# Kernel optimization log

Hardware: AMD Instinct MI355X
Metric: run time of the kernel (lower is better)

The kernel has to match this reference:

```python
import jax, jax.numpy as jnp
import numpy as np

BATCH, T, H, S, P, NH = 4, 2048, 1024, 64, 64, 8
HD = H // NH

def setup_inputs() -> dict:
    key = jax.random.key(0)
    ks = jax.random.split(key, 16)
    sH = 1.0 / np.sqrt(H)
    d = {}
    d["builder_state"] = jax.random.normal(ks[0], (BATCH, T, H), jnp.float32)
    d["base_state"] = jax.random.normal(ks[1], (BATCH, T, H), jnp.float32)
    d["input_ids"] = jax.random.randint(ks[2], (BATCH, T), 0, 32000)
    d["program_probs"] = jax.random.uniform(ks[3], (BATCH, T, P), jnp.float32)
    # SSM params (scaled from raw randn for numerical stability of the 2048-step recurrence)
    d["A"] = jax.random.normal(ks[4], (S, S), jnp.float32) * (0.5 / np.sqrt(S))
    d["Bmat"] = jax.random.normal(ks[5], (H, S), jnp.float32) * sH
    d["Cmat"] = jax.random.normal(ks[6], (S, H), jnp.float32) * (1.0 / np.sqrt(S))
    d["W_in"] = jax.random.normal(ks[7], (H, H), jnp.float32) * sH
    d["b_in"] = jnp.zeros((H,), jnp.float32)
    d["W_qkv"] = jax.random.normal(ks[8], (3 * H, H), jnp.float32) * sH
    d["b_qkv"] = jnp.zeros((3 * H,), jnp.float32)
    d["W_o"] = jax.random.normal(ks[9], (H, H), jnp.float32) * sH
    d["b_o"] = jnp.zeros((H,), jnp.float32)
    d["W_prog"] = jax.random.normal(ks[10], (H, P), jnp.float32) * (1.0 / np.sqrt(P))
    d["b_prog"] = jnp.zeros((H,), jnp.float32)
    d["g1"] = jnp.ones((H,), jnp.float32); d["beta1"] = jnp.zeros((H,), jnp.float32)
    d["g2"] = jnp.ones((H,), jnp.float32); d["beta2"] = jnp.zeros((H,), jnp.float32)
    return d

def _layernorm(x, g, b):
    mu = jnp.mean(x, axis=-1, keepdims=True)
    var = jnp.mean((x - mu) ** 2, axis=-1, keepdims=True)
    return (x - mu) * jax.lax.rsqrt(var + 1e-5) * g + b

def _mha(q_in, kv_in, W_qkv, b_qkv, W_o, b_o):
    Wq, Wk, Wv = jnp.split(W_qkv, 3, axis=0)
    bq, bk, bv = jnp.split(b_qkv, 3, axis=0)
    def heads(x, W, b):  # [B,T,H] -> [B,NH,T,HD]
        y = x @ W.T + b
        return y.reshape(y.shape[0], y.shape[1], NH, HD).transpose(0, 2, 1, 3)
    q, k, v = heads(q_in, Wq, bq), heads(kv_in, Wk, bk), heads(kv_in, Wv, bv)
    scores = jnp.einsum('bhqd,bhkd->bhqk', q, k) * (1.0 / np.sqrt(HD))
    attn = jax.nn.softmax(scores, axis=-1)
    out = jnp.einsum('bhqk,bhkd->bhqd', attn, v)
    out = out.transpose(0, 2, 1, 3).reshape(q_in.shape)
    return out @ W_o.T + b_o

def reference(builder_state, base_state, input_ids, program_probs,
              A, Bmat, Cmat, W_in, b_in, W_qkv, b_qkv, W_o, b_o,
              W_prog, b_prog, g1, beta1, g2, beta2):
    # cross-attention sublayer (norm1 shared between builder and base states)
    residual = builder_state
    x = _layernorm(builder_state, g1, beta1)
    base_n = _layernorm(base_state, g1, beta1)
    x = residual + _mha(x, base_n, W_qkv, b_qkv, W_o, b_o)
    # SSM sublayer: state_{t} = silu(A @ state_{t-1}) + B^T u_t ; y_t = state_t @ C
    residual = x
    xn = _layernorm(x, g2, beta2)
    U = (xn @ W_in.T + b_in) @ Bmat            # [B,T,S] precomputed input drive
    def step(s, u_t):                           # s: [B,S], u_t: [B,S]
        s = jax.nn.silu(s @ A.T) + u_t
        return s, s
    _, states = jax.lax.scan(step, jnp.zeros((builder_state.shape[0], S), U.dtype),
                             U.transpose(1, 0, 2))  # states: [T,B,S]
    ssm_out = jnp.einsum('tbs,sh->bth', states, Cmat)
    x = residual + ssm_out
    # program modulation
    mod = program_probs.mean(axis=1) @ W_prog.T + b_prog   # [B,H]
    return x + mod[:, None, :]
```

## Files before the change

### kernel.cpp

```cpp
#include <hip/hip_runtime.h>
#include <cstdint>
#include <cstddef>

typedef unsigned short u16;
typedef short bf16x8 __attribute__((ext_vector_type(8)));
typedef float f32x4 __attribute__((ext_vector_type(4)));
typedef u16 u16x4 __attribute__((ext_vector_type(4)));
typedef u16 u16x8 __attribute__((ext_vector_type(8)));

#define DEVFN static __device__ __forceinline__

DEVFN u16 f32_to_bf16(float f){
  unsigned u = __float_as_uint(f);
  u += 0x7fffu + ((u >> 16) & 1u);
  return (u16)(u >> 16);
}

DEVFN f32x4 mfma16(bf16x8 a, bf16x8 b, f32x4 c){
  return __builtin_amdgcn_mfma_f32_16x16x32_bf16(a, b, c, 0, 0, 0);
}

DEVFN void gload_lds16(const void* g, void* l){
  __builtin_amdgcn_global_load_lds(
      (const __attribute__((address_space(1))) void*)g,
      (__attribute__((address_space(3))) void*)l, 16, 0, 0);
}

__global__ __launch_bounds__(256,1) void prep_kernel(
    const float* __restrict__ W_qkv, const float* __restrict__ W_o,
    const float* __restrict__ Cm, const float* __restrict__ W_in,
    const float* __restrict__ Bm, const float* __restrict__ b_in,
    const float* __restrict__ pp,
    u16* __restrict__ Wq16, u16* __restrict__ Wo16, u16* __restrict__ CmT,
    u16* __restrict__ WcT, float* __restrict__ ub, float* __restrict__ partial)
{
  const int blk = blockIdx.x;
  if (blk < 1024){
    for (int i = blk*256 + threadIdx.x; i < 786432; i += 1024*256){
      float4 v = ((const float4*)W_qkv)[i];
      u16x4 o; o[0]=f32_to_bf16(v.x); o[1]=f32_to_bf16(v.y); o[2]=f32_to_bf16(v.z); o[3]=f32_to_bf16(v.w);
      ((u16x4*)Wq16)[i] = o;
    }
  } else if (blk < 1280){
    for (int i = (blk-1024)*256 + threadIdx.x; i < 262144; i += 256*256){
      float4 v = ((const float4*)W_o)[i];
      u16x4 o; o[0]=f32_to_bf16(v.x); o[1]=f32_to_bf16(v.y); o[2]=f32_to_bf16(v.z); o[3]=f32_to_bf16(v.w);
      ((u16x4*)Wo16)[i] = o;
    }
  } else if (blk < 1536){
    int i = (blk-1280)*256 + threadIdx.x;
    int h = i >> 6, s = i & 63;
    CmT[i] = f32_to_bf16(Cm[s*1024 + h]);
  } else if (blk < 1792){
    int b2 = blk - 1536;
    const int kl = threadIdx.x & 63, sl = threadIdx.x >> 6;
    const int k = ((b2 & 15) << 6) + kl;
    const int s = ((b2 >> 4) << 2) + sl;
    float a = 0.f;
#pragma unroll 8
    for (int jj = 0; jj < 1024; jj++) a = fmaf(W_in[jj*1024 + k], Bm[jj*64 + s], a);
    WcT[s*1024 + k] = f32_to_bf16(a);
  } else if (blk == 1792){
    if (threadIdx.x < 64){
      const int s = threadIdx.x;
      float a = 0.f;
      for (int jj = 0; jj < 1024; jj++) a = fmaf(b_in[jj], Bm[jj*64 + s], a);
      ub[s] = a;
    }
  } else {
    const int idx = blk - 1793;
    const int c = idx & 31, b = idx >> 5, t = threadIdx.x;
    const int p = t & 63, g = t >> 6;
    const float* basep = pp + (size_t)b*2048*64 + (size_t)c*64*64;
    float s = 0.f;
#pragma unroll
    for (int i = g*16; i < g*16 + 16; i++) s += basep[i*64 + p];
    __shared__ float red[256];
    red[t] = s;
    __syncthreads();
    if (t < 64) partial[(b*32 + c)*64 + t] = (red[t] + red[64+t]) + (red[128+t] + red[192+t]);
  }
}

DEVFN void ln_row(const float* __restrict__ srcrow, u16* __restrict__ dstrow,
                  const float* __restrict__ g, const float* __restrict__ beta, int t)
{
  const float4 v = ((const float4*)srcrow)[t];
  float s1 = v.x+v.y+v.z+v.w;
  float s2 = v.x*v.x+v.y*v.y+v.z*v.z+v.w*v.w;
#pragma unroll
  for (int off = 32; off > 0; off >>= 1){ s1 += __shfl_xor(s1, off); s2 += __shfl_xor(s2, off); }
  __shared__ float w1[4], w2[4];
  if ((t & 63) == 0){ w1[t>>6] = s1; w2[t>>6] = s2; }
  __syncthreads();
  s1 = (w1[0]+w1[1])+(w1[2]+w1[3]);
  s2 = (w2[0]+w2[1])+(w2[2]+w2[3]);
  const float mean = s1*(1.f/1024.f);
  const float var  = s2*(1.f/1024.f) - mean*mean;
  const float rstd = rsqrtf(var + 1e-5f);
  const float4 gv = ((const float4*)g)[t];
  const float4 bv = ((const float4*)beta)[t];
  u16x4 o;
  o[0] = f32_to_bf16((v.x-mean)*rstd*gv.x + bv.x);
  o[1] = f32_to_bf16((v.y-mean)*rstd*gv.y + bv.y);
  o[2] = f32_to_bf16((v.z-mean)*rstd*gv.z + bv.z);
  o[3] = f32_to_bf16((v.w-mean)*rstd*gv.w + bv.w);
  *(u16x4*)&dstrow[t*4] = o;
}

__global__ __launch_bounds__(256,1) void ln_bf16_kernel(
    const float* __restrict__ src, u16* __restrict__ dst,
    const float* __restrict__ g, const float* __restrict__ beta)
{
  const int row = blockIdx.x;
  ln_row(src + (size_t)row*1024, dst + (size_t)row*1024, g, beta, threadIdx.x);
}

__global__ __launch_bounds__(256,1) void ln2x_bf16_kernel(
    const float* __restrict__ src0, u16* __restrict__ dst0,
    const float* __restrict__ src1, u16* __restrict__ dst1,
    const float* __restrict__ g, const float* __restrict__ beta)
{
  int row = blockIdx.x;
  if (row < 8192) ln_row(src0 + (size_t)row*1024, dst0 + (size_t)row*1024, g, beta, threadIdx.x);
  else { row -= 8192; ln_row(src1 + (size_t)row*1024, dst1 + (size_t)row*1024, g, beta, threadIdx.x); }
}

template<int BM,int BN,int WM,int WN,int MT,int NT,int EPI>
__global__ __launch_bounds__(256,1) void gemm_bt(
    const u16* __restrict__ Ag, const u16* __restrict__ Bg,
    void* __restrict__ Cout, const float* __restrict__ bias,
    const float* __restrict__ resid, const float* __restrict__ modv,
    int M, int N, int K)
{
  static_assert(BM == WM*MT*16 && BN == WN*NT*16 && WM*WN == 4, "tile config");
  __shared__ u16 As[BM*64];
  __shared__ u16 Bs[BN*64];
  const int t = threadIdx.x;
  const int lane = t & 63, wave = t >> 6;
  const int wm = wave / WN, wn = wave % WN;
  const int lrow = lane & 15, lq = lane >> 4;
  const int m0 = blockIdx.y * BM, n0 = blockIdx.x * BN;

  f32x4 acc[MT][NT];
#pragma unroll
  for (int i = 0; i < MT; i++)
#pragma unroll
    for (int j = 0; j < NT; j++){ acc[i][j][0]=0.f; acc[i][j][1]=0.f; acc[i][j][2]=0.f; acc[i][j][3]=0.f; }

  for (int kt = 0; kt < K; kt += 64){
#pragma unroll
    for (int i = 0; i < BM/32; i++){
      int idx = (i*4 + wave)*64 + lane;
      int r = idx >> 3, s = idx & 7;
      int c = s ^ (r & 7);
      gload_lds16(&Ag[(size_t)(m0 + r)*K + kt + c*8], &As[(size_t)(i*4 + wave)*64*8]);
    }
#pragma unroll
    for (int i = 0; i < BN/32; i++){
      int idx = (i*4 + wave)*64 + lane;
      int r = idx >> 3, s = idx & 7;
      int c = s ^ (r & 7);
      gload_lds16(&Bg[(size_t)(n0 + r)*K + kt + c*8], &Bs[(size_t)(i*4 + wave)*64*8]);
    }
    __syncthreads();
#pragma unroll
    for (int kk = 0; kk < 2; kk++){
      bf16x8 af[MT], bfr[NT];
      const int sl = (kk*4 + lq) ^ (lrow & 7);
#pragma unroll
      for (int mt = 0; mt < MT; mt++)
        af[mt] = *(const bf16x8*)&As[(wm*MT*16 + mt*16 + lrow)*64 + sl*8];
#pragma unroll
      for (int nt = 0; nt < NT; nt++)
        bfr[nt] = *(const bf16x8*)&Bs[(wn*NT*16 + nt*16 + lrow)*64 + sl*8];
#pragma unroll
      for (int mt = 0; mt < MT; mt++)
#pragma unroll
        for (int nt = 0; nt < NT; nt++)
          acc[mt][nt] = mfma16(af[mt], bfr[nt], acc[mt][nt]);
    }
    __syncthreads();
  }
  const int rb = m0 + wm*MT*16;
  const int cb = n0 + wn*NT*16;
#pragma unroll
  for (int mt = 0; mt < MT; mt++){
#pragma unroll
    for (int nt = 0; nt < NT; nt++){
#pragma unroll
      for (int r = 0; r < 4; r++){
        int row = rb + mt*16 + lq*4 + r;
        int col = cb + nt*16 + lrow;
        float v = acc[mt][nt][r];
        if (EPI & 2) v += bias[col];
        if (EPI & 4) v += resid[(size_t)row*N + col];
        if (EPI & 8) v += modv[(row >> 11)*1024 + col];
        if (EPI & 1) ((u16*)Cout)[(size_t)row*N + col] = f32_to_bf16(v);
        else         ((float*)Cout)[(size_t)row*N + col] = v;
      }
    }
  }
}

__global__ __launch_bounds__(256,1) void gemm_qkv(
    const u16* __restrict__ QNa, const u16* __restrict__ KVNa,
    const u16* __restrict__ Wq, u16* __restrict__ Qb, u16* __restrict__ KVb,
    const float* __restrict__ bias)
{
  const int bid = blockIdx.x;
  const u16* Ag; const u16* Bg; u16* Cout; const float* bp;
  int N, m0, n0; float scale;
  if (bid < 512){
    Ag = QNa; Bg = Wq; Cout = Qb; bp = bias; N = 1024;
    m0 = (bid >> 3) * 128; n0 = (bid & 7) * 128;
    scale = 0.08838834764831845f * 1.4426950408889634f;
  } else {
    int b2 = bid - 512;
    Ag = KVNa; Bg = Wq + 1024*1024; Cout = KVb; bp = bias + 1024; N = 2048;
    m0 = (b2 >> 4) * 128; n0 = (b2 & 15) * 128;
    scale = 1.0f;
  }
  const int K = 1024;
  __shared__ u16 As[128*64];
  __shared__ u16 Bs[128*64];
  const int t = threadIdx.x;
  const int lane = t & 63, wave = t >> 6;
  const int wm = wave >> 1, wn = wave & 1;
  const int lrow = lane & 15, lq = lane >> 4;

  f32x4 acc[4][4];
#pragma unroll
  for (int i = 0; i < 4; i++)
#pragma unroll
    for (int j = 0; j < 4; j++){ acc[i][j][0]=0.f; acc[i][j][1]=0.f; acc[i][j][2]=0.f; acc[i][j][3]=0.f; }

  for (int kt = 0; kt < K; kt += 64){
#pragma unroll
    for (int i = 0; i < 4; i++){
      int idx = (i*4 + wave)*64 + lane;
      int r = idx >> 3, s = idx & 7;
      int c = s ^ (r & 7);
      gload_lds16(&Ag[(size_t)(m0 + r)*K + kt + c*8], &As[(size_t)(i*4 + wave)*64*8]);
    }
#pragma unroll
    for (int i = 0; i < 4; i++){
      int idx = (i*4 + wave)*64 + lane;
      int r = idx >> 3, s = idx & 7;
      int c = s ^ (r & 7);
      gload_lds16(&Bg[(size_t)(n0 + r)*K + kt + c*8], &Bs[(size_t)(i*4 + wave)*64*8]);
    }
    __syncthreads();
#pragma unroll
    for (int kk = 0; kk < 2; kk++){
      bf16x8 af[4], bfr[4];
      const int sl = (kk*4 + lq) ^ (lrow & 7);
#pragma unroll
      for (int mt = 0; mt < 4; mt++)
        af[mt] = *(const bf16x8*)&As[(wm*64 + mt*16 + lrow)*64 + sl*8];
#pragma unroll
      for (int nt = 0; nt < 4; nt++)
        bfr[nt] = *(const bf16x8*)&Bs[(wn*64 + nt*16 + lrow)*64 + sl*8];
#pragma unroll
      for (int mt = 0; mt < 4; mt++)
#pragma unroll
        for (int nt = 0; nt < 4; nt++)
          acc[mt][nt] = mfma16(af[mt], bfr[nt], acc[mt][nt]);
    }
    __syncthreads();
  }
  const int rb = m0 + wm*64;
  const int cb = n0 + wn*64;
#pragma unroll
  for (int mt = 0; mt < 4; mt++){
#pragma unroll
    for (int nt = 0; nt < 4; nt++){
#pragma unroll
      for (int r = 0; r < 4; r++){
        int row = rb + mt*16 + lq*4 + r;
        int col = cb + nt*16 + lrow;
        float v = (acc[mt][nt][r] + bp[col]) * scale;
        Cout[(size_t)row*N + col] = f32_to_bf16(v);
      }
    }
  }
}

__global__ __launch_bounds__(512,1) void flash_attn(
    const u16* __restrict__ Qb, const u16* __restrict__ KVb, u16* __restrict__ Ob)
{
  __shared__ u16 Ks[64*128];
  __shared__ unsigned Vt2[128*34];
  __shared__ u16 Ps[8][16*68];
  const int t = threadIdx.x;
  const int lane = t & 63, wave = t >> 6;
  const int lrow = lane & 15, lq = lane >> 4;
  const int b = blockIdx.y >> 3, h = blockIdx.y & 7;
  const int q0 = blockIdx.x * 128;

  bf16x8 qf[4];
  {
    int grow = b*2048 + q0 + wave*16 + lrow;
#pragma unroll
    for (int ks = 0; ks < 4; ks++)
      qf[ks] = *(const bf16x8*)&Qb[(size_t)grow*1024 + h*128 + ks*32 + lq*8];
  }
  float lsum[4] = {0.f,0.f,0.f,0.f};
  f32x4 Oa[8];
#pragma unroll
  for (int i = 0; i < 8; i++){ Oa[i][0]=0.f; Oa[i][1]=0.f; Oa[i][2]=0.f; Oa[i][3]=0.f; }

  const int key_k = t >> 3, cg = t & 7;
  const int kp = t & 31, dg = t >> 5;

  const size_t KSTEP = (size_t)64*2048;
  const u16* Kpg = &KVb[(size_t)(b*2048 + key_k)*2048 + h*128];
  const u16* Vpg = &KVb[(size_t)(b*2048 + kp*2)*2048 + h*128 + 1024 + dg*8];

  u16x8 kreg[2];
  u16x8 vreg[2];

#pragma unroll
  for (int i = 0; i < 2; i++) kreg[i] = *(const u16x8*)&Kpg[(cg*2+i)*8];
  vreg[0] = *(const u16x8*)&Vpg[0];
  vreg[1] = *(const u16x8*)&Vpg[2048];
#pragma unroll
  for (int i = 0; i < 2; i++){
    int ch = cg*2 + i;
    int ph = ch ^ (key_k & 7);
    *(u16x8*)&Ks[key_k*128 + ph*8] = kreg[i];
  }
#pragma unroll
  for (int jj = 0; jj < 8; jj++)
    Vt2[(dg*8+jj)*34 + kp] = (unsigned)vreg[0][jj] | ((unsigned)vreg[1][jj] << 16);

  for (int kt = 0; kt < 32; kt++){
    __syncthreads();
    if (kt < 31){
      const u16* kpg = Kpg + (size_t)(kt+1)*KSTEP;
#pragma unroll
      for (int i = 0; i < 2; i++) kreg[i] = *(const u16x8*)&kpg[(cg*2+i)*8];
      const u16* vg = Vpg + (size_t)(kt+1)*KSTEP;
      vreg[0] = *(const u16x8*)&vg[0];
      vreg[1] = *(const u16x8*)&vg[2048];
    }

    f32x4 sacc[4];
    __builtin_amdgcn_s_setprio(1);
#pragma unroll
    for (int nt = 0; nt < 4; nt++){
      f32x4 a; a[0]=0.f; a[1]=0.f; a[2]=0.f; a[3]=0.f;
#pragma unroll
      for (int ks = 0; ks < 4; ks++){
        int ph = (ks*4 + lq) ^ (lrow & 7);
        bf16x8 kf = *(const bf16x8*)&Ks[(nt*16+lrow)*128 + ph*8];
        a = mfma16(qf[ks], kf, a);
      }
      sacc[nt] = a;
    }
    __builtin_amdgcn_s_setprio(0);
#pragma unroll
    for (int nt = 0; nt < 4; nt++)
#pragma unroll
      for (int r = 0; r < 4; r++){
        float p = exp2f(sacc[nt][r]);
        lsum[r] += p;
        Ps[wave][(lq*4+r)*68 + nt*16 + lrow] = f32_to_bf16(p);
      }
    __builtin_amdgcn_s_setprio(1);
#pragma unroll
    for (int ks2 = 0; ks2 < 2; ks2++){
      bf16x8 pa;
      ((u16x4*)&pa)[0] = *(const u16x4*)&Ps[wave][lrow*68 + ks2*32 + lq*8];
      ((u16x4*)&pa)[1] = *(const u16x4*)&Ps[wave][lrow*68 + ks2*32 + lq*8 + 4];
#pragma unroll
      for (int nt2 = 0; nt2 < 8; nt2++){
        bf16x8 vf;
        int dwoff = (nt2*16+lrow)*34 + ks2*16 + lq*4;
        ((uint2*)&vf)[0] = *(const uint2*)&Vt2[dwoff];
        ((uint2*)&vf)[1] = *(const uint2*)&Vt2[dwoff+2];
        Oa[nt2] = mfma16(pa, vf, Oa[nt2]);
      }
    }
    __builtin_amdgcn_s_setprio(0);
    __syncthreads();
    if (kt < 31){
#pragma unroll
      for (int i = 0; i < 2; i++){
        int ch = cg*2 + i;
        int ph = ch ^ (key_k & 7);
        *(u16x8*)&Ks[key_k*128 + ph*8] = kreg[i];
      }
#pragma unroll
      for (int jj = 0; jj < 8; jj++)
        Vt2[(dg*8+jj)*34 + kp] = (unsigned)vreg[0][jj] | ((unsigned)vreg[1][jj] << 16);
    }
  }
#pragma unroll
  for (int r = 0; r < 4; r++){
#pragma unroll
    for (int off = 1; off < 16; off <<= 1) lsum[r] += __shfl_xor(lsum[r], off);
  }
  float inv[4];
#pragma unroll
  for (int r = 0; r < 4; r++) inv[r] = 1.0f / lsum[r];
  const int growb = b*2048 + q0 + wave*16;
#pragma unroll
  for (int nt2 = 0; nt2 < 8; nt2++)
#pragma unroll
    for (int r = 0; r < 4; r++){
      float o = Oa[nt2][r]*inv[r];
      Ob[(size_t)(growb + lq*4 + r)*1024 + h*128 + nt2*16 + lrow] = f32_to_bf16(o);
    }
}

__global__ __launch_bounds__(64,1) void scan_chunk_kernel(
    const float* __restrict__ U, const float* __restrict__ A, u16* __restrict__ S,
    const float* __restrict__ partial, const float* __restrict__ Wp,
    const float* __restrict__ bp, float* __restrict__ mo)
{
  const int b = blockIdx.y, c = blockIdx.x, j = threadIdx.x;
  if (c == 64){
    float s = 0.f;
#pragma unroll
    for (int cc = 0; cc < 32; cc++) s += partial[(b*32 + cc)*64 + j];
    __shared__ float pms[64];
    pms[j] = s * (1.f/2048.f);
    __syncthreads();
    for (int jo = 0; jo < 16; jo++){
      int hc = jo*64 + j;
      float a = bp[hc];
#pragma unroll 8
      for (int q = 0; q < 64; q++) a = fmaf(pms[q], Wp[hc*64+q], a);
      mo[b*1024 + hc] = a;
    }
    return;
  }
  float Ar[64];
#pragma unroll
  for (int k = 0; k < 64; k++) Ar[k] = A[j*64 + k];
  const float* Ub = U + (size_t)b*2048*64;
  u16* Sb = S + (size_t)b*2048*64;
  const int tout = c*32;
  const int tend = tout + 32;
  int t0 = tout - 48; if (t0 < 0) t0 = 0;
  __shared__ float sbuf[2][64];
  sbuf[0][j] = 0.f;
  __syncthreads();
  float unext = Ub[t0*64 + j];
  const float NLOG2E = -1.4426950408889634f;
  for (int t = t0; t < tend; t++){
    const int cur = (t - t0) & 1;
    f32x4 sv[16];
#pragma unroll
    for (int r = 0; r < 16; r++) sv[r] = *((const f32x4*)&sbuf[cur][r*4]);
    float u = unext;
    int tn = t + 1; if (tn >= tend) tn = tend - 1;
    unext = Ub[tn*64 + j];
    float a0=0.f, a1=0.f, a2=0.f, a3=0.f;
#pragma unroll
    for (int r = 0; r < 16; r++){
      a0 = fmaf(Ar[4*r+0], sv[r][0], a0);
      a1 = fmaf(Ar[4*r+1], sv[r][1], a1);
      a2 = fmaf(Ar[4*r+2], sv[r][2], a2);
      a3 = fmaf(Ar[4*r+3], sv[r][3], a3);
    }
    float y = (a0+a1)+(a2+a3);
    float e = exp2f(y*NLOG2E);
    float s = fmaf(y, __builtin_amdgcn_rcpf(1.f + e), u);
    sbuf[cur^1][j] = s;
    if (t >= tout) Sb[t*64 + j] = f32_to_bf16(s);
  }
}

extern "C" void kernel_launch(void* const* d_in, const int* in_sizes, int n_in,
                              void* d_out, int out_size, void* d_ws, size_t ws_size,
                              hipStream_t stream)
{
  (void)in_sizes; (void)n_in; (void)out_size; (void)ws_size;
  const float* builder = (const float*)d_in[0];
  const float* base    = (const float*)d_in[1];
  const float* pp      = (const float*)d_in[3];
  const float* Amat    = (const float*)d_in[4];
  const float* Bmat    = (const float*)d_in[5];
  const float* Cmat    = (const float*)d_in[6];
  const float* W_in    = (const float*)d_in[7];
  const float* b_in    = (const float*)d_in[8];
  const float* W_qkv   = (const float*)d_in[9];
  const float* b_qkv   = (const float*)d_in[10];
  const float* W_o     = (const float*)d_in[11];
  const float* b_o     = (const float*)d_in[12];
  const float* W_prog  = (const float*)d_in[13];
  const float* b_prog  = (const float*)d_in[14];
  const float* g1      = (const float*)d_in[15];
  const float* beta1   = (const float*)d_in[16];
  const float* g2      = (const float*)d_in[17];
  const float* beta2   = (const float*)d_in[18];
  float* out = (float*)d_out;

  char* ws = (char*)d_ws;
  const size_t MB = (size_t)1 << 20;
  u16*   Qb   = (u16*)  (ws + 0*MB);
  u16*   KVb  = (u16*)  (ws + 16*MB);
  float* Xf   = (float*)(ws + 48*MB);
  u16*   QN   = (u16*)  (ws + 80*MB);
  u16*   KVN  = (u16*)  (ws + 96*MB);
  u16*   Wq16 = (u16*)  (ws + 112*MB);
  u16*   Wo16 = (u16*)  (ws + 118*MB);
  u16*   WcT  = (u16*)  (ws + 120*MB);
  u16*   CmT  = (u16*)  (ws + 120*MB + 256*1024);
  float* Uf   = (float*)(ws + 121*MB);
  u16*   Sb   = (u16*)  (ws + 123*MB);
  float* ub   = (float*)(ws + 124*MB);
  float* modv = (float*)(ws + 124*MB + 8192);
  float* ppart= (float*)(ws + 124*MB + 32768);

  prep_kernel<<<1921,256,0,stream>>>(W_qkv, W_o, Cmat, W_in, Bmat, b_in, pp,
                                     Wq16, Wo16, CmT, WcT, ub, ppart);

  ln2x_bf16_kernel<<<16384,256,0,stream>>>(builder, QN, base, KVN, g1, beta1);

  gemm_qkv<<<1536,256,0,stream>>>(QN, KVN, Wq16, Qb, KVb, b_qkv);

  flash_attn<<<dim3(16,32),512,0,stream>>>(Qb, KVb, QN);

  gemm_bt<128,128,2,2,4,4,6><<<dim3(8,64),256,0,stream>>>(QN, Wo16, Xf, b_o, builder, nullptr, 8192,1024,1024);

  ln_bf16_kernel<<<8192,256,0,stream>>>(Xf, KVN, g2, beta2);

  gemm_bt<64,64,2,2,2,2,2><<<dim3(1,128),256,0,stream>>>(KVN, WcT, Uf, ub, nullptr, nullptr, 8192,64,1024);

  scan_chunk_kernel<<<dim3(65,4),64,0,stream>>>(Uf, Amat, Sb, ppart, W_prog, b_prog, modv);

  gemm_bt<128,128,2,2,4,4,12><<<dim3(8,64),256,0,stream>>>(Sb, CmT, out, nullptr, Xf, modv, 8192,1024,64);
}
```

Measured before the change: 511.9 us.

## Rewrite flash attention with 32x32 MFMA and in-register P via permlane swap

```diff
diff --git a/kernel.cpp b/kernel.cpp
--- a/kernel.cpp
+++ b/kernel.cpp
@@ -5,6 +5,7 @@
 typedef unsigned short u16;
 typedef short bf16x8 __attribute__((ext_vector_type(8)));
 typedef float f32x4 __attribute__((ext_vector_type(4)));
+typedef float f32x16 __attribute__((ext_vector_type(16)));
 typedef u16 u16x4 __attribute__((ext_vector_type(4)));
 typedef u16 u16x8 __attribute__((ext_vector_type(8)));
 
@@ -18,6 +19,10 @@
 
 DEVFN f32x4 mfma16(bf16x8 a, bf16x8 b, f32x4 c){
   return __builtin_amdgcn_mfma_f32_16x16x32_bf16(a, b, c, 0, 0, 0);
+}
+
+DEVFN f32x16 mfma32(bf16x8 a, bf16x8 b, f32x16 c){
+  return __builtin_amdgcn_mfma_f32_32x32x16_bf16(a, b, c, 0, 0, 0);
 }
 
 DEVFN void gload_lds16(const void* g, void* l){
@@ -286,131 +291,162 @@
   }
 }
 
-__global__ __launch_bounds__(512,1) void flash_attn(
+__global__ __launch_bounds__(256,1) void flash_attn(
     const u16* __restrict__ Qb, const u16* __restrict__ KVb, u16* __restrict__ Ob)
 {
   __shared__ u16 Ks[64*128];
   __shared__ unsigned Vt2[128*34];
-  __shared__ u16 Ps[8][16*68];
   const int t = threadIdx.x;
   const int lane = t & 63, wave = t >> 6;
-  const int lrow = lane & 15, lq = lane >> 4;
+  const int l31 = lane & 31, hi = lane >> 5;
   const int b = blockIdx.y >> 3, h = blockIdx.y & 7;
   const int q0 = blockIdx.x * 128;
 
-  bf16x8 qf[4];
+  bf16x8 qf[8];
   {
-    int grow = b*2048 + q0 + wave*16 + lrow;
-#pragma unroll
-    for (int ks = 0; ks < 4; ks++)
-      qf[ks] = *(const bf16x8*)&Qb[(size_t)grow*1024 + h*128 + ks*32 + lq*8];
-  }
-  float lsum[4] = {0.f,0.f,0.f,0.f};
-  f32x4 Oa[8];
-#pragma unroll
-  for (int i = 0; i < 8; i++){ Oa[i][0]=0.f; Oa[i][1]=0.f; Oa[i][2]=0.f; Oa[i][3]=0.f; }
-
-  const int key_k = t >> 3, cg = t & 7;
+    const size_t qbase = (size_t)(b*2048 + q0 + wave*32 + l31)*1024 + h*128 + hi*8;
+#pragma unroll
+    for (int f = 0; f < 8; f++)
+      qf[f] = *(const bf16x8*)&Qb[qbase + f*16];
+  }
+  float lsum = 0.f;
+  f32x16 Oa[4];
+#pragma unroll
+  for (int i = 0; i < 4; i++)
+#pragma unroll
+    for (int r = 0; r < 16; r++) Oa[i][r] = 0.f;
+
+  const int key_k = t >> 2, cg = t & 3;
   const int kp = t & 31, dg = t >> 5;
-
   const size_t KSTEP = (size_t)64*2048;
   const u16* Kpg = &KVb[(size_t)(b*2048 + key_k)*2048 + h*128];
-  const u16* Vpg = &KVb[(size_t)(b*2048 + kp*2)*2048 + h*128 + 1024 + dg*8];
-
-  u16x8 kreg[2];
-  u16x8 vreg[2];
-
-#pragma unroll
-  for (int i = 0; i < 2; i++) kreg[i] = *(const u16x8*)&Kpg[(cg*2+i)*8];
+  const u16* Vpg = &KVb[(size_t)(b*2048 + kp*2)*2048 + h*128 + 1024 + dg*16];
+
+  u16x8 kreg[4];
+  u16x8 vreg[4];
+
+#pragma unroll
+  for (int i = 0; i < 4; i++) kreg[i] = *(const u16x8*)&Kpg[(cg*4+i)*8];
   vreg[0] = *(const u16x8*)&Vpg[0];
-  vreg[1] = *(const u16x8*)&Vpg[2048];
-#pragma unroll
-  for (int i = 0; i < 2; i++){
-    int ch = cg*2 + i;
+  vreg[1] = *(const u16x8*)&Vpg[8];
+  vreg[2] = *(const u16x8*)&Vpg[2048];
+  vreg[3] = *(const u16x8*)&Vpg[2048+8];
+#pragma unroll
+  for (int i = 0; i < 4; i++){
+    int ch = cg*4 + i;
     int ph = ch ^ (key_k & 7);
     *(u16x8*)&Ks[key_k*128 + ph*8] = kreg[i];
   }
 #pragma unroll
-  for (int jj = 0; jj < 8; jj++)
-    Vt2[(dg*8+jj)*34 + kp] = (unsigned)vreg[0][jj] | ((unsigned)vreg[1][jj] << 16);
+  for (int jj = 0; jj < 8; jj++){
+    Vt2[(dg*16+jj)*34 + kp]   = (unsigned)vreg[0][jj] | ((unsigned)vreg[2][jj] << 16);
+    Vt2[(dg*16+8+jj)*34 + kp] = (unsigned)vreg[1][jj] | ((unsigned)vreg[3][jj] << 16);
+  }
 
   for (int kt = 0; kt < 32; kt++){
     __syncthreads();
     if (kt < 31){
       const u16* kpg = Kpg + (size_t)(kt+1)*KSTEP;
 #pragma unroll
-      for (int i = 0; i < 2; i++) kreg[i] = *(const u16x8*)&kpg[(cg*2+i)*8];
+      for (int i = 0; i < 4; i++) kreg[i] = *(const u16x8*)&kpg[(cg*4+i)*8];
       const u16* vg = Vpg + (size_t)(kt+1)*KSTEP;
       vreg[0] = *(const u16x8*)&vg[0];
-      vreg[1] = *(const u16x8*)&vg[2048];
-    }
-
-    f32x4 sacc[4];
+      vreg[1] = *(const u16x8*)&vg[8];
+      vreg[2] = *(const u16x8*)&vg[2048];
+      vreg[3] = *(const u16x8*)&vg[2048+8];
+    }
+
+    unsigned w[16];
+    {
+      f32x16 a;
+#pragma unroll
+      for (int r = 0; r < 16; r++) a[r] = 0.f;
+      __builtin_amdgcn_s_setprio(1);
+#pragma unroll
+      for (int f = 0; f < 8; f++){
+        int ph = (f*2 + hi) ^ (l31 & 7);
+        bf16x8 kf = *(const bf16x8*)&Ks[l31*128 + ph*8];
+        a = mfma32(kf, qf[f], a);
+      }
+      __builtin_amdgcn_s_setprio(0);
+#pragma unroll
+      for (int r2 = 0; r2 < 8; r2++){
+        float p0 = exp2f(a[2*r2]);
+        float p1 = exp2f(a[2*r2+1]);
+        lsum += p0 + p1;
+        asm("v_cvt_pk_bf16_f32 %0, %1, %2" : "=v"(w[r2]) : "v"(p0), "v"(p1));
+      }
+    }
+    {
+      f32x16 a;
+#pragma unroll
+      for (int r = 0; r < 16; r++) a[r] = 0.f;
+      __builtin_amdgcn_s_setprio(1);
+#pragma unroll
+      for (int f = 0; f < 8; f++){
+        int ph = (f*2 + hi) ^ (l31 & 7);
+        bf16x8 kf = *(const bf16x8*)&Ks[(32 + l31)*128 + ph*8];
+        a = mfma32(kf, qf[f], a);
+      }
+      __builtin_amdgcn_s_setprio(0);
+#pragma unroll
+      for (int r2 = 0; r2 < 8; r2++){
+        float p0 = exp2f(a[2*r2]);
+        float p1 = exp2f(a[2*r2+1]);
+        lsum += p0 + p1;
+        asm("v_cvt_pk_bf16_f32 %0, %1, %2" : "=v"(w[8+r2]) : "v"(p0), "v"(p1));
+      }
+    }
+#pragma unroll
+    for (int g = 0; g < 4; g++){
+      asm("v_permlane32_swap_b32 %0, %1" : "+v"(w[g*4+0]), "+v"(w[g*4+2]));
+      asm("v_permlane32_swap_b32 %0, %1" : "+v"(w[g*4+1]), "+v"(w[g*4+3]));
+    }
     __builtin_amdgcn_s_setprio(1);
 #pragma unroll
-    for (int nt = 0; nt < 4; nt++){
-      f32x4 a; a[0]=0.f; a[1]=0.f; a[2]=0.f; a[3]=0.f;
-#pragma unroll
-      for (int ks = 0; ks < 4; ks++){
-        int ph = (ks*4 + lq) ^ (lrow & 7);
-        bf16x8 kf = *(const bf16x8*)&Ks[(nt*16+lrow)*128 + ph*8];
-        a = mfma16(qf[ks], kf, a);
-      }
-      sacc[nt] = a;
-    }
-    __builtin_amdgcn_s_setprio(0);
-#pragma unroll
-    for (int nt = 0; nt < 4; nt++)
-#pragma unroll
-      for (int r = 0; r < 4; r++){
-        float p = exp2f(sacc[nt][r]);
-        lsum[r] += p;
-        Ps[wave][(lq*4+r)*68 + nt*16 + lrow] = f32_to_bf16(p);
-      }
-    __builtin_amdgcn_s_setprio(1);
-#pragma unroll
-    for (int ks2 = 0; ks2 < 2; ks2++){
+    for (int kg = 0; kg < 4; kg++){
       bf16x8 pa;
-      ((u16x4*)&pa)[0] = *(const u16x4*)&Ps[wave][lrow*68 + ks2*32 + lq*8];
-      ((u16x4*)&pa)[1] = *(const u16x4*)&Ps[wave][lrow*68 + ks2*32 + lq*8 + 4];
-#pragma unroll
-      for (int nt2 = 0; nt2 < 8; nt2++){
+      ((unsigned*)&pa)[0] = w[kg*4+0];
+      ((unsigned*)&pa)[1] = w[kg*4+1];
+      ((unsigned*)&pa)[2] = w[kg*4+2];
+      ((unsigned*)&pa)[3] = w[kg*4+3];
+#pragma unroll
+      for (int db = 0; db < 4; db++){
         bf16x8 vf;
-        int dwoff = (nt2*16+lrow)*34 + ks2*16 + lq*4;
+        int dwoff = (db*32 + l31)*34 + kg*8 + hi*4;
         ((uint2*)&vf)[0] = *(const uint2*)&Vt2[dwoff];
         ((uint2*)&vf)[1] = *(const uint2*)&Vt2[dwoff+2];
-        Oa[nt2] = mfma16(pa, vf, Oa[nt2]);
+        Oa[db] = mfma32(pa, vf, Oa[db]);
       }
     }
     __builtin_amdgcn_s_setprio(0);
     __syncthreads();
     if (kt < 31){
 #pragma unroll
-      for (int i = 0; i < 2; i++){
-        int ch = cg*2 + i;
+      for (int i = 0; i < 4; i++){
+        int ch = cg*4 + i;
         int ph = ch ^ (key_k & 7);
         *(u16x8*)&Ks[key_k*128 + ph*8] = kreg[i];
       }
 #pragma unroll
-      for (int jj = 0; jj < 8; jj++)
-        Vt2[(dg*8+jj)*34 + kp] = (unsigned)vreg[0][jj] | ((unsigned)vreg[1][jj] << 16);
-    }
-  }
-#pragma unroll
-  for (int r = 0; r < 4; r++){
-#pragma unroll
-    for (int off = 1; off < 16; off <<= 1) lsum[r] += __shfl_xor(lsum[r], off);
-  }
-  float inv[4];
-#pragma unroll
-  for (int r = 0; r < 4; r++) inv[r] = 1.0f / lsum[r];
-  const int growb = b*2048 + q0 + wave*16;
-#pragma unroll
-  for (int nt2 = 0; nt2 < 8; nt2++)
-#pragma unroll
-    for (int r = 0; r < 4; r++){
-      float o = Oa[nt2][r]*inv[r];
-      Ob[(size_t)(growb + lq*4 + r)*1024 + h*128 + nt2*16 + lrow] = f32_to_bf16(o);
+      for (int jj = 0; jj < 8; jj++){
+        Vt2[(dg*16+jj)*34 + kp]   = (unsigned)vreg[0][jj] | ((unsigned)vreg[2][jj] << 16);
+        Vt2[(dg*16+8+jj)*34 + kp] = (unsigned)vreg[1][jj] | ((unsigned)vreg[3][jj] << 16);
+      }
+    }
+  }
+  lsum += __shfl_xor(lsum, 32);
+  float inv = 1.0f / lsum;
+  float invq[16];
+#pragma unroll
+  for (int r = 0; r < 16; r++) invq[r] = __shfl(inv, (r&3) + 8*(r>>2) + 4*hi);
+  const int growb = b*2048 + q0 + wave*32;
+#pragma unroll
+  for (int db = 0; db < 4; db++)
+#pragma unroll
+    for (int r = 0; r < 16; r++){
+      int qrow = (r&3) + 8*(r>>2) + 4*hi;
+      Ob[(size_t)(growb + qrow)*1024 + h*128 + db*32 + l31] = f32_to_bf16(Oa[db][r]*invq[r]);
     }
 }
 
@@ -522,7 +558,7 @@
 
   gemm_qkv<<<1536,256,0,stream>>>(QN, KVN, Wq16, Qb, KVb, b_qkv);
 
-  flash_attn<<<dim3(16,32),512,0,stream>>>(Qb, KVb, QN);
+  flash_attn<<<dim3(16,32),256,0,stream>>>(Qb, KVb, QN);
 
   gemm_bt<128,128,2,2,4,4,6><<<dim3(8,64),256,0,stream>>>(QN, Wo16, Xf, b_o, builder, nullptr, 8192,1024,1024);
 
```

New measurement: 567.9 us. 1.11x slower.
